# Kernel tuning notes

Measured on AMD Instinct MI355X. Metric: run time of the kernel, lower is better.

The kernel has to match this reference:

```python
import jax, jax.numpy as jnp
import numpy as np

B, T, E = 2, 2048, 1024
H = 16            # num_heads (global in source repo)
D = E // H        # head_len
LN_EPS = 1e-5


def setup_inputs() -> dict:
    key = jax.random.key(0)
    ks = jax.random.split(key, 12)
    s = lambda fan_in: 1.0 / np.sqrt(fan_in)
    return {
        "x":     jax.random.normal(ks[0], (B, T, E), jnp.float32),
        "ln1_g": jnp.ones((E,), jnp.float32),
        "ln1_b": jnp.zeros((E,), jnp.float32),
        "Wq":    jax.random.normal(ks[1], (E, E), jnp.float32) * s(E),
        "Wk":    jax.random.normal(ks[2], (E, E), jnp.float32) * s(E),
        "Wv":    jax.random.normal(ks[3], (E, E), jnp.float32) * s(E),
        "Wo":    jax.random.normal(ks[4], (E, E), jnp.float32) * s(E),
        "bo":    jnp.zeros((E,), jnp.float32),
        "ln2_g": jnp.ones((E,), jnp.float32),
        "ln2_b": jnp.zeros((E,), jnp.float32),
        "W1":    jax.random.normal(ks[5], (E, 4 * E), jnp.float32) * s(E),
        "b1":    jnp.zeros((4 * E,), jnp.float32),
        "W2":    jax.random.normal(ks[6], (4 * E, E), jnp.float32) * s(4 * E),
        "b2":    jnp.zeros((E,), jnp.float32),
    }


def _layernorm(x, g, b):
    mu = jnp.mean(x, axis=-1, keepdims=True)
    var = jnp.mean(jnp.square(x - mu), axis=-1, keepdims=True)
    return (x - mu) * jax.lax.rsqrt(var + LN_EPS) * g + b


def _attention(x, Wq, Wk, Wv, Wo, bo):
    b, t, e = x.shape
    q = (x @ Wq).reshape(b, t, H, D)
    k = (x @ Wk).reshape(b, t, H, D)
    v = (x @ Wv).reshape(b, t, H, D)
    scores = jnp.einsum("bqhd,bkhd->bhqk", q, k) / np.sqrt(D).astype(np.float32)
    causal = jnp.tril(jnp.ones((t, t), bool))
    scores = jnp.where(causal, scores, -jnp.inf)
    attn = jax.nn.softmax(scores, axis=-1)
    out = jnp.einsum("bhqk,bkhd->bqhd", attn, v).reshape(b, t, e)
    return out @ Wo + bo


def reference(x, ln1_g, ln1_b, Wq, Wk, Wv, Wo, bo, ln2_g, ln2_b, W1, b1, W2, b2):
    # pre-norm attention + residual (dropout=0 / eval mode)
    x = x + _attention(_layernorm(x, ln1_g, ln1_b), Wq, Wk, Wv, Wo, bo)
    # pre-norm MLP + residual
    h = _layernorm(x, ln2_g, ln2_b)
    h = jax.nn.relu(h @ W1 + b1) @ W2 + b2
    return x + h
```

## Files before the change

### kernel.cpp

```cpp
#include <hip/hip_runtime.h>
#include <cmath>
#include <cstdint>
#include <cstddef>

typedef __bf16 bf16_t;
typedef __bf16 bf16x8 __attribute__((ext_vector_type(8)));
typedef float  f32x4  __attribute__((ext_vector_type(4)));

#define B_   2
#define T_   2048
#define E_   1024
#define H_   16
#define D_   64
#define FF_  4096
#define NROW (B_ * T_)
#define QS_  (3 * E_)
#define NTI  (T_ / 64)

__global__ __launch_bounds__(256) void ln_kernel(
    const float* __restrict__ x, const float* __restrict__ g,
    const float* __restrict__ bta, bf16_t* __restrict__ out)
{
    int row = blockIdx.x;
    int tid = threadIdx.x;
    const float4* xr = (const float4*)(x + (size_t)row * E_);
    float4 v = xr[tid];
    float s  = v.x + v.y + v.z + v.w;
    float ss = v.x * v.x + v.y * v.y + v.z * v.z + v.w * v.w;
#pragma unroll
    for (int off = 32; off; off >>= 1) {
        s  += __shfl_xor(s, off);
        ss += __shfl_xor(ss, off);
    }
    __shared__ float red[8];
    int wave = tid >> 6, lane = tid & 63;
    if (lane == 0) { red[wave] = s; red[4 + wave] = ss; }
    __syncthreads();
    s  = red[0] + red[1] + red[2] + red[3];
    ss = red[4] + red[5] + red[6] + red[7];
    float mu   = s * (1.0f / E_);
    float var  = ss * (1.0f / E_) - mu * mu;
    float rstd = rsqrtf(var + 1e-5f);
    float4 gv = ((const float4*)g)[tid];
    float4 bv = ((const float4*)bta)[tid];
    union { bf16_t h[4]; ushort4 u; } pk;
    pk.h[0] = (bf16_t)((v.x - mu) * rstd * gv.x + bv.x);
    pk.h[1] = (bf16_t)((v.y - mu) * rstd * gv.y + bv.y);
    pk.h[2] = (bf16_t)((v.z - mu) * rstd * gv.z + bv.z);
    pk.h[3] = (bf16_t)((v.w - mu) * rstd * gv.w + bv.w);
    ((ushort4*)(out + (size_t)row * E_))[tid] = pk.u;
}

__global__ __launch_bounds__(256) void ln_reduce2(
    const float* __restrict__ p, const float* __restrict__ bias,
    const float* __restrict__ resid, float* __restrict__ x1,
    const float* __restrict__ g, const float* __restrict__ bta,
    bf16_t* __restrict__ out)
{
    int row = blockIdx.x;
    int tid = threadIdx.x;
    size_t off = (size_t)row * E_;
    float4 v0 = ((const float4*)(p + off))[tid];
    float4 v1 = ((const float4*)(p + (size_t)NROW * E_ + off))[tid];
    float4 bb = ((const float4*)bias)[tid];
    float4 rr = ((const float4*)(resid + off))[tid];
    float4 v;
    v.x = v0.x + v1.x + bb.x + rr.x;
    v.y = v0.y + v1.y + bb.y + rr.y;
    v.z = v0.z + v1.z + bb.z + rr.z;
    v.w = v0.w + v1.w + bb.w + rr.w;
    ((float4*)(x1 + off))[tid] = v;
    float s  = v.x + v.y + v.z + v.w;
    float ss = v.x * v.x + v.y * v.y + v.z * v.z + v.w * v.w;
#pragma unroll
    for (int o = 32; o; o >>= 1) {
        s  += __shfl_xor(s, o);
        ss += __shfl_xor(ss, o);
    }
    __shared__ float red[8];
    int wave = tid >> 6, lane = tid & 63;
    if (lane == 0) { red[wave] = s; red[4 + wave] = ss; }
    __syncthreads();
    s  = red[0] + red[1] + red[2] + red[3];
    ss = red[4] + red[5] + red[6] + red[7];
    float mu   = s * (1.0f / E_);
    float var  = ss * (1.0f / E_) - mu * mu;
    float rstd = rsqrtf(var + 1e-5f);
    float4 gv = ((const float4*)g)[tid];
    float4 bv = ((const float4*)bta)[tid];
    union { bf16_t h[4]; ushort4 u; } pk;
    pk.h[0] = (bf16_t)((v.x - mu) * rstd * gv.x + bv.x);
    pk.h[1] = (bf16_t)((v.y - mu) * rstd * gv.y + bv.y);
    pk.h[2] = (bf16_t)((v.z - mu) * rstd * gv.z + bv.z);
    pk.h[3] = (bf16_t)((v.w - mu) * rstd * gv.w + bv.w);
    ((ushort4*)(out + off))[tid] = pk.u;
}

__global__ __launch_bounds__(256) void add_reduce4(
    const float* __restrict__ p, const float* __restrict__ bias,
    const float* __restrict__ resid, float* __restrict__ out)
{
    int row = blockIdx.x;
    int tid = threadIdx.x;
    size_t off = (size_t)row * E_;
    const size_t MN = (size_t)NROW * E_;
    float4 v0 = ((const float4*)(p + off))[tid];
    float4 v1 = ((const float4*)(p + MN + off))[tid];
    float4 v2 = ((const float4*)(p + 2 * MN + off))[tid];
    float4 v3 = ((const float4*)(p + 3 * MN + off))[tid];
    float4 bb = ((const float4*)bias)[tid];
    float4 rr = ((const float4*)(resid + off))[tid];
    float4 v;
    v.x = (v0.x + v1.x) + (v2.x + v3.x) + bb.x + rr.x;
    v.y = (v0.y + v1.y) + (v2.y + v3.y) + bb.y + rr.y;
    v.z = (v0.z + v1.z) + (v2.z + v3.z) + bb.z + rr.z;
    v.w = (v0.w + v1.w) + (v2.w + v3.w) + bb.w + rr.w;
    ((float4*)(out + off))[tid] = v;
}

__global__ __launch_bounds__(256) void transpose_all(
    const float* __restrict__ Wq, const float* __restrict__ Wk,
    const float* __restrict__ Wv, const float* __restrict__ Wo,
    const float* __restrict__ W1, const float* __restrict__ W2,
    bf16_t* __restrict__ wqkv, bf16_t* __restrict__ wot,
    bf16_t* __restrict__ w1t, bf16_t* __restrict__ w2t)
{
    int l = blockIdx.x;
    const float* W; bf16_t* Wt; int K, N, bx, by;
    if (l < 4096) {
        int seg = l >> 10, r = l & 1023;
        K = E_; N = E_; bx = r & 31; by = r >> 5;
        if      (seg == 0) { W = Wq; Wt = wqkv; }
        else if (seg == 1) { W = Wk; Wt = wqkv + (size_t)E_ * E_; }
        else if (seg == 2) { W = Wv; Wt = wqkv + (size_t)2 * E_ * E_; }
        else               { W = Wo; Wt = wot; }
    } else if (l < 8192) {
        int r = l - 4096; K = E_; N = FF_; bx = r & 127; by = r >> 7;
        W = W1; Wt = w1t;
    } else {
        int r = l - 8192; K = FF_; N = E_; bx = r & 31; by = r >> 5;
        W = W2; Wt = w2t;
    }
    __shared__ float t[32][33];
    int n0 = bx * 32, k0 = by * 32;
    int tx = threadIdx.x & 31, ty = threadIdx.x >> 5;
#pragma unroll
    for (int i = 0; i < 4; ++i)
        t[ty + i * 8][tx] = W[(size_t)(k0 + ty + i * 8) * N + n0 + tx];
    __syncthreads();
#pragma unroll
    for (int i = 0; i < 4; ++i)
        Wt[(size_t)(n0 + ty + i * 8) * K + k0 + tx] = (bf16_t)t[tx][ty + i * 8];
}

#define BM 128
#define BN 128
#define BK 64

__device__ __forceinline__ void gload16(const bf16_t* g, bf16_t* l)
{
    __builtin_amdgcn_global_load_lds(
        (const __attribute__((address_space(1))) void*)g,
        (__attribute__((address_space(3))) void*)l, 16, 0, 0);
}

__global__ __launch_bounds__(256) void gemm_bt(
    const bf16_t* __restrict__ A, const bf16_t* __restrict__ Bt,
    const float* __restrict__ bias, const float* __restrict__ resid,
    void* __restrict__ Cout, bf16_t* __restrict__ vt_out,
    int M, int N, int K, int lda, int ldb,
    int has_bias, int do_relu, int has_resid, int out_bf16)
{
    __shared__ __attribute__((aligned(16))) bf16_t As[BM * BK];
    __shared__ __attribute__((aligned(16))) bf16_t Bs[BN * BK];
    int tid  = threadIdx.x;
    int lane = tid & 63, wave = tid >> 6;
    int m0 = blockIdx.x * BM, n0 = blockIdx.y * BN;
    int wm = (wave & 1) * 64, wn = (wave >> 1) * 64;
    int koff = blockIdx.z * K;
    f32x4 acc[4][4];
#pragma unroll
    for (int i = 0; i < 4; ++i)
#pragma unroll
        for (int j = 0; j < 4; ++j) acc[i][j] = (f32x4){0.f, 0.f, 0.f, 0.f};

    const int kq = (lane >> 4) * 8;
    const int ml = lane & 15;

    int srow = wave * 32 + (lane >> 3);
    int scol = (lane & 7) * 8;
    const bf16_t* Ag = A  + (size_t)(m0 + srow) * lda + koff + scol;
    const bf16_t* Bg = Bt + (size_t)(n0 + srow) * ldb + koff + scol;
    bf16_t* Asw = &As[wave * 32 * BK];
    bf16_t* Bsw = &Bs[wave * 32 * BK];
    int niter = K / BK;

#pragma unroll
    for (int j = 0; j < 4; ++j) {
        gload16(Ag + (size_t)j * 8 * lda, Asw + j * 8 * BK);
        gload16(Bg + (size_t)j * 8 * ldb, Bsw + j * 8 * BK);
    }

    for (int it = 0; it < niter; ++it) {
        __syncthreads();
#pragma unroll
        for (int ks = 0; ks < 2; ++ks) {
            bf16x8 af[4], bfr[4];
#pragma unroll
            for (int mi = 0; mi < 4; ++mi)
                af[mi] = *(const bf16x8*)&As[(wm + mi * 16 + ml) * BK + ks * 32 + kq];
#pragma unroll
            for (int ni = 0; ni < 4; ++ni)
                bfr[ni] = *(const bf16x8*)&Bs[(wn + ni * 16 + ml) * BK + ks * 32 + kq];
#pragma unroll
            for (int mi = 0; mi < 4; ++mi)
#pragma unroll
                for (int ni = 0; ni < 4; ++ni)
                    acc[mi][ni] = __builtin_amdgcn_mfma_f32_16x16x32_bf16(
                        af[mi], bfr[ni], acc[mi][ni], 0, 0, 0);
        }
        if (it + 1 < niter) {
            __syncthreads();
            int k0 = (it + 1) * BK;
#pragma unroll
            for (int j = 0; j < 4; ++j) {
                gload16(Ag + k0 + (size_t)j * 8 * lda, Asw + j * 8 * BK);
                gload16(Bg + k0 + (size_t)j * 8 * ldb, Bsw + j * 8 * BK);
            }
        }
    }

    int r4 = (lane >> 4) * 4;
    if (gridDim.z > 1) {
        float* P = (float*)Cout + (size_t)blockIdx.z * M * N;
#pragma unroll
        for (int mi = 0; mi < 4; ++mi)
#pragma unroll
            for (int ni = 0; ni < 4; ++ni) {
                int col = n0 + wn + ni * 16 + ml;
#pragma unroll
                for (int r = 0; r < 4; ++r) {
                    int row = m0 + wm + mi * 16 + r4 + r;
                    P[(size_t)row * N + col] = acc[mi][ni][r];
                }
            }
        return;
    }
#pragma unroll
    for (int mi = 0; mi < 4; ++mi) {
#pragma unroll
        for (int ni = 0; ni < 4; ++ni) {
            int col = n0 + wn + ni * 16 + ml;
            float bval = has_bias ? bias[col] : 0.0f;
#pragma unroll
            for (int r = 0; r < 4; ++r) {
                int row = m0 + wm + mi * 16 + r4 + r;
                float v = acc[mi][ni][r] + bval;
                if (do_relu)   v = fmaxf(v, 0.0f);
                if (has_resid) v += resid[(size_t)row * N + col];
                if (out_bf16)
                    ((bf16_t*)Cout)[(size_t)row * N + col] = (bf16_t)v;
                else
                    ((float*)Cout)[(size_t)row * N + col] = v;
            }
        }
    }
}


__device__ __forceinline__ void g256_stage_half(
    const bf16_t* gbase, int ldg, bf16_t* lhalf, int wave, int lane)
{
    int r = lane >> 3, c = lane & 7;
    int sc = (c ^ r) * 8;
#pragma unroll
    for (int j = 0; j < 2; ++j) {
        const bf16_t* src = gbase + (size_t)(wave * 8 + j * 64 + r) * ldg + sc;
        bf16_t* dst = lhalf + (wave * 8 + j * 64) * 64;
        __builtin_amdgcn_global_load_lds(
            (const __attribute__((address_space(1))) void*)src,
            (__attribute__((address_space(3))) void*)dst, 16, 0, 0);
    }
}

__device__ __forceinline__ bf16x8 g256_frag(const bf16_t* half, int row, int kb)
{
    return *(const bf16x8*)((const char*)half + row * 128 + (kb ^ ((row & 7) << 4)));
}

template<int FP, bool DO_BFR>
__device__ __forceinline__ void g256_reads(
    const bf16_t* Ahx, const bf16_t* Bhx,
    bf16x8 (&af)[2][2], bf16x8 (&bfr)[4][2],
    int ml, int kq16, int brow0)
{
    if (DO_BFR) {
#pragma unroll
        for (int ni = 0; ni < 4; ++ni) {
            bfr[ni][0] = g256_frag(Bhx, brow0 + ni * 16 + ml, kq16);
            bfr[ni][1] = g256_frag(Bhx, brow0 + ni * 16 + ml, 64 + kq16);
        }
    }
#pragma unroll
    for (int i = 0; i < 2; ++i) {
        af[i][0] = g256_frag(Ahx, (2 * FP + i) * 16 + ml, kq16);
        af[i][1] = g256_frag(Ahx, (2 * FP + i) * 16 + ml, 64 + kq16);
    }
}

template<int FP>
__device__ __forceinline__ void g256_mfma(
    const bf16x8 (&af)[2][2], const bf16x8 (&bfr)[4][2], f32x4 (&acc)[8][4])
{
    __builtin_amdgcn_s_setprio(1);
#pragma unroll
    for (int i = 0; i < 2; ++i)
#pragma unroll
        for (int ni = 0; ni < 4; ++ni)
#pragma unroll
            for (int ks = 0; ks < 2; ++ks)
                acc[2 * FP + i][ni] = __builtin_amdgcn_mfma_f32_16x16x32_bf16(
                    af[i][ks], bfr[ni][ks], acc[2 * FP + i][ni], 0, 0, 0);
    __builtin_amdgcn_s_setprio(0);
}

#define AHALF(t, h) (ldsr + ((((t) & 1) * 4 + (h)) * (128 * 64)))
#define BHALF(t, h) (ldsr + ((((t) & 1) * 4 + 2 + (h)) * (128 * 64)))
#define STG_A(t, h) g256_stage_half(Ab + (size_t)((h) * 128) * lda + (t) * 64, lda, AHALF(t, h), wave, lane)
#define STG_B(t, h) g256_stage_half(Bb + (size_t)((h) * 128) * ldb + (t) * 64, ldb, BHALF(t, h), wave, lane)
#define SBAR() __builtin_amdgcn_s_barrier()

__global__ __launch_bounds__(512, 2) void gemm256(
    const bf16_t* __restrict__ A, const bf16_t* __restrict__ Bt,
    const float* __restrict__ bias,
    void* __restrict__ Cout, bf16_t* __restrict__ vt_out,
    int M, int N, int K, int lda, int ldb,
    int has_bias, int do_relu, int split)
{
    extern __shared__ __attribute__((aligned(16))) bf16_t ldsr[];
    int tid = threadIdx.x, lane = tid & 63, wave = tid >> 6;
    int m0 = blockIdx.x * 256, n0 = blockIdx.y * 256;
    int koff = blockIdx.z * K;
    int ml = lane & 15, kq16 = (lane >> 4) * 16, r4 = (lane >> 4) * 4;
    int wr = (wave >> 2) * 128, wc = (wave & 3) * 64;
    int brow0 = (wave & 1) * 64;

    const bf16_t* Ab = A  + (size_t)m0 * lda + koff;
    const bf16_t* Bb = Bt + (size_t)n0 * ldb + koff;

    const bf16_t* A0 = AHALF(0, wave >> 2);
    const bf16_t* A1 = AHALF(1, wave >> 2);
    const bf16_t* B0 = BHALF(0, (wave & 3) >> 1);
    const bf16_t* B1 = BHALF(1, (wave & 3) >> 1);

    f32x4 acc[8][4];
#pragma unroll
    for (int i = 0; i < 8; ++i)
#pragma unroll
        for (int j = 0; j < 4; ++j) acc[i][j] = (f32x4){0.f, 0.f, 0.f, 0.f};
    bf16x8 bfr[4][2];

    STG_B(0, 0); STG_B(0, 1);
    STG_A(0, 0); STG_A(0, 1);
    STG_B(1, 0); STG_B(1, 1);
    asm volatile("s_waitcnt vmcnt(4)" ::: "memory");
    SBAR();

    int NIT2 = K / 128;
    for (int it = 0; it < NIT2; ++it) {
        bool last = (it == NIT2 - 1);
        int t1 = 2 * it + 1, t2 = 2 * it + 2, t3 = 2 * it + 3;
        bf16x8 af[2][2];

        g256_reads<0, true>(A0, B0, af, bfr, ml, kq16, brow0);
        STG_A(t1, 0);
        SBAR();
        g256_mfma<0>(af, bfr, acc);
        SBAR();

        g256_reads<1, false>(A0, B0, af, bfr, ml, kq16, brow0);
        STG_A(t1, 1);
        SBAR();
        g256_mfma<1>(af, bfr, acc);
        SBAR();

        g256_reads<2, false>(A0, B0, af, bfr, ml, kq16, brow0);
        if (!last) STG_B(t2, 0);
        SBAR();
        g256_mfma<2>(af, bfr, acc);
        SBAR();

        g256_reads<3, false>(A0, B0, af, bfr, ml, kq16, brow0);
        if (!last) STG_B(t2, 1);
        SBAR();
        g256_mfma<3>(af, bfr, acc);
        if (last) asm volatile("s_waitcnt vmcnt(0)" ::: "memory");
        else      asm volatile("s_waitcnt vmcnt(4)" ::: "memory");
        SBAR();

        g256_reads<0, true>(A1, B1, af, bfr, ml, kq16, brow0);
        if (!last) STG_A(t2, 0);
        SBAR();
        g256_mfma<0>(af, bfr, acc);
        SBAR();

        g256_reads<1, false>(A1, B1, af, bfr, ml, kq16, brow0);
        if (!last) STG_A(t2, 1);
        SBAR();
        g256_mfma<1>(af, bfr, acc);
        SBAR();

        g256_reads<2, false>(A1, B1, af, bfr, ml, kq16, brow0);
        if (!last) STG_B(t3, 0);
        SBAR();
        g256_mfma<2>(af, bfr, acc);
        SBAR();

        g256_reads<3, false>(A1, B1, af, bfr, ml, kq16, brow0);
        if (!last) STG_B(t3, 1);
        SBAR();
        g256_mfma<3>(af, bfr, acc);
        if (!last) asm volatile("s_waitcnt vmcnt(4)" ::: "memory");
        SBAR();
    }

    if (split > 1) {
        float* P = (float*)Cout + (size_t)blockIdx.z * M * N;
#pragma unroll
        for (int mi = 0; mi < 8; ++mi)
#pragma unroll
            for (int ni = 0; ni < 4; ++ni) {
                int col = n0 + wc + ni * 16 + ml;
#pragma unroll
                for (int r = 0; r < 4; ++r) {
                    int row = m0 + wr + mi * 16 + r4 + r;
                    P[(size_t)row * N + col] = acc[mi][ni][r];
                }
            }
        return;
    }
    if (vt_out && n0 >= 2 * E_) {
#pragma unroll
        for (int mi = 0; mi < 8; ++mi)
#pragma unroll
            for (int ni = 0; ni < 4; ++ni) {
                int vcol = n0 + wc + ni * 16 + ml - 2 * E_;
                int h = vcol >> 6, d = vcol & 63;
                int row0 = m0 + wr + mi * 16 + r4;
                int b = row0 >> 11, t = row0 & (T_ - 1);
                union { bf16_t h4[4]; uint2 u; } pk;
#pragma unroll
                for (int r = 0; r < 4; ++r) pk.h4[r] = (bf16_t)acc[mi][ni][r];
                *(uint2*)&vt_out[((size_t)(b * H_ + h) * D_ + d) * T_ + t] = pk.u;
            }
        return;
    }
#pragma unroll
    for (int mi = 0; mi < 8; ++mi) {
#pragma unroll
        for (int ni = 0; ni < 4; ++ni) {
            int col = n0 + wc + ni * 16 + ml;
            float bval = has_bias ? bias[col] : 0.0f;
#pragma unroll
            for (int r = 0; r < 4; ++r) {
                int row = m0 + wr + mi * 16 + r4 + r;
                float v = acc[mi][ni][r] + bval;
                if (do_relu) v = fmaxf(v, 0.0f);
                ((bf16_t*)Cout)[(size_t)row * N + col] = (bf16_t)v;
            }
        }
    }
}

#define PSTR 72

struct TileState {
    f32x4 acc[4];
    float m1, l1;
};

__device__ __forceinline__ void tile_update(
    const bf16x8 kf[2][4], const bf16x8 vf[2][4], const bf16x8 qf[2],
    TileState& st, bf16_t* PsW, int ml, int r4, int kq8,
    bool diag, int ch, int qrow)
{
    f32x4 s[4];
#pragma unroll
    for (int nt = 0; nt < 4; ++nt) {
        s[nt] = (f32x4){0.f, 0.f, 0.f, 0.f};
#pragma unroll
        for (int ks = 0; ks < 2; ++ks)
            s[nt] = __builtin_amdgcn_mfma_f32_16x16x32_bf16(kf[ks][nt], qf[ks], s[nt], 0, 0, 0);
    }
    if (diag) {
#pragma unroll
        for (int nt = 0; nt < 4; ++nt)
#pragma unroll
            for (int r = 0; r < 4; ++r)
                if (ch * 64 + nt * 16 + r4 + r > qrow) s[nt][r] = -INFINITY;
    }
    float mx = -INFINITY;
#pragma unroll
    for (int nt = 0; nt < 4; ++nt)
#pragma unroll
        for (int r = 0; r < 4; ++r) mx = fmaxf(mx, s[nt][r]);
    mx = fmaxf(mx, __shfl_xor(mx, 16));
    mx = fmaxf(mx, __shfl_xor(mx, 32));
    float mn = fmaxf(st.m1, mx);
    float al = __expf(st.m1 - mn);
    st.m1 = mn;
    float sum = 0.f;
#pragma unroll
    for (int nt = 0; nt < 4; ++nt)
#pragma unroll
        for (int r = 0; r < 4; ++r) {
            float p = __expf(s[nt][r] - mn);
            s[nt][r] = p;
            sum += p;
        }
    sum += __shfl_xor(sum, 16);
    sum += __shfl_xor(sum, 32);
    st.l1 = st.l1 * al + sum;
#pragma unroll
    for (int dt = 0; dt < 4; ++dt)
#pragma unroll
        for (int r = 0; r < 4; ++r) st.acc[dt][r] *= al;

#pragma unroll
    for (int nt = 0; nt < 4; ++nt) {
        union { bf16_t h[4]; uint2 u; } pk;
#pragma unroll
        for (int r = 0; r < 4; ++r) pk.h[r] = (bf16_t)s[nt][r];
        *(uint2*)&PsW[ml * PSTR + nt * 16 + r4] = pk.u;
    }
#pragma unroll
    for (int ks = 0; ks < 2; ++ks) {
        bf16x8 pf = *(const bf16x8*)&PsW[ml * PSTR + ks * 32 + kq8];
#pragma unroll
        for (int dt = 0; dt < 4; ++dt)
            st.acc[dt] = __builtin_amdgcn_mfma_f32_16x16x32_bf16(vf[ks][dt], pf, st.acc[dt], 0, 0, 0);
    }
}

__global__ __launch_bounds__(256) void attn_mfma(
    const bf16_t* __restrict__ Qp, const bf16_t* __restrict__ Kp,
    const bf16_t* __restrict__ Vt, bf16_t* __restrict__ O)
{
    __shared__ __attribute__((aligned(16))) bf16_t Ks[2][64 * PSTR];
    __shared__ __attribute__((aligned(16))) bf16_t Vts[2][64 * PSTR];
    __shared__ __attribute__((aligned(16))) bf16_t Ps[4][16 * PSTR];

    int tid = threadIdx.x, lane = tid & 63, wave = tid >> 6;
    int ml  = lane & 15;
    int kq8 = (lane >> 4) * 8;
    int r4  = (lane >> 4) * 4;
    int bh = blockIdx.y, b = bh >> 4, h = bh & 15;
    size_t qk_base = (size_t)b * T_ * QS_ + h * D_;
    size_t vt_base = (size_t)bh * D_ * T_;
    size_t o_base  = (size_t)b * T_ * E_ + h * D_;

    int lo = blockIdx.x, hi = NTI - 1 - blockIdx.x;
    int qlo = lo * 64 + wave * 16;
    int qhi = hi * 64 + wave * 16;

    bf16x8 qfl[2], qfh[2];
#pragma unroll
    for (int ks = 0; ks < 2; ++ks) {
        bf16x8 a = *(const bf16x8*)&Qp[qk_base + (size_t)(qlo + ml) * QS_ + ks * 32 + kq8];
        bf16x8 c = *(const bf16x8*)&Qp[qk_base + (size_t)(qhi + ml) * QS_ + ks * 32 + kq8];
#pragma unroll
        for (int j = 0; j < 8; ++j) {
            a[j] = (bf16_t)((float)a[j] * 0.125f);
            c[j] = (bf16_t)((float)c[j] * 0.125f);
        }
        qfl[ks] = a; qfh[ks] = c;
    }

    TileState stl, sth;
#pragma unroll
    for (int dt = 0; dt < 4; ++dt) {
        stl.acc[dt] = (f32x4){0.f, 0.f, 0.f, 0.f};
        sth.acc[dt] = (f32x4){0.f, 0.f, 0.f, 0.f};
    }
    stl.m1 = -INFINITY; stl.l1 = 0.f;
    sth.m1 = -INFINITY; sth.l1 = 0.f;

    int r0 = tid >> 3, c0 = (tid & 7) * 8;
    int nch = hi + 1;

    {
        const bf16_t* kb = &Kp[qk_base + (size_t)r0 * QS_ + c0];
        const bf16_t* vb = &Vt[vt_base + (size_t)r0 * T_ + c0];
        uint4 k0v = *(const uint4*)kb;
        uint4 k1v = *(const uint4*)(kb + (size_t)32 * QS_);
        uint4 v0v = *(const uint4*)vb;
        uint4 v1v = *(const uint4*)(vb + (size_t)32 * T_);
        *(uint4*)&Ks[0][r0 * PSTR + c0]         = k0v;
        *(uint4*)&Ks[0][(r0 + 32) * PSTR + c0]  = k1v;
        *(uint4*)&Vts[0][r0 * PSTR + c0]        = v0v;
        *(uint4*)&Vts[0][(r0 + 32) * PSTR + c0] = v1v;
    }

    for (int ch = 0; ch < nch; ++ch) {
        int cur = ch & 1, nxt = cur ^ 1;
        __syncthreads();

        uint4 nk0, nk1, nv0, nv1;
        bool pf = (ch + 1 < nch);
        if (pf) {
            const bf16_t* kb = &Kp[qk_base + (size_t)((ch + 1) * 64 + r0) * QS_ + c0];
            const bf16_t* vb = &Vt[vt_base + (size_t)r0 * T_ + (ch + 1) * 64 + c0];
            nk0 = *(const uint4*)kb;
            nk1 = *(const uint4*)(kb + (size_t)32 * QS_);
            nv0 = *(const uint4*)vb;
            nv1 = *(const uint4*)(vb + (size_t)32 * T_);
        }

        bf16x8 kf[2][4], vf[2][4];
#pragma unroll
        for (int ks = 0; ks < 2; ++ks)
#pragma unroll
            for (int nt = 0; nt < 4; ++nt) {
                kf[ks][nt] = *(const bf16x8*)&Ks[cur][(nt * 16 + ml) * PSTR + ks * 32 + kq8];
                vf[ks][nt] = *(const bf16x8*)&Vts[cur][(nt * 16 + ml) * PSTR + ks * 32 + kq8];
            }

        tile_update(kf, vf, qfh, sth, Ps[wave], ml, r4, kq8,
                    ch == hi, ch, qhi + ml);
        if (ch <= lo)
            tile_update(kf, vf, qfl, stl, Ps[wave], ml, r4, kq8,
                        ch == lo, ch, qlo + ml);

        if (pf) {
            *(uint4*)&Ks[nxt][r0 * PSTR + c0]         = nk0;
            *(uint4*)&Ks[nxt][(r0 + 32) * PSTR + c0]  = nk1;
            *(uint4*)&Vts[nxt][r0 * PSTR + c0]        = nv0;
            *(uint4*)&Vts[nxt][(r0 + 32) * PSTR + c0] = nv1;
        }
    }

#pragma unroll
    for (int t = 0; t < 2; ++t) {
        TileState& st = t ? stl : sth;
        int qw = t ? qlo : qhi;
        float inv = 1.0f / st.l1;
#pragma unroll
        for (int dt = 0; dt < 4; ++dt) {
            union { bf16_t h[4]; uint2 u; } pk;
#pragma unroll
            for (int r = 0; r < 4; ++r) pk.h[r] = (bf16_t)(st.acc[dt][r] * inv);
            *(uint2*)&Ps[wave][ml * PSTR + dt * 16 + r4] = pk.u;
        }
        int row = lane >> 2, seg = (lane & 3) * 16;
        bf16x8 o0 = *(const bf16x8*)&Ps[wave][row * PSTR + seg];
        bf16x8 o1 = *(const bf16x8*)&Ps[wave][row * PSTR + seg + 8];
        size_t gp = o_base + (size_t)(qw + row) * E_ + seg;
        *(bf16x8*)&O[gp]     = o0;
        *(bf16x8*)&O[gp + 8] = o1;
    }
}

extern "C" void kernel_launch(void* const* d_in, const int* in_sizes, int n_in,
                              void* d_out, int out_size, void* d_ws, size_t ws_size,
                              hipStream_t stream)
{
    const float* x    = (const float*)d_in[0];
    const float* ln1g = (const float*)d_in[1];
    const float* ln1b = (const float*)d_in[2];
    const float* Wq   = (const float*)d_in[3];
    const float* Wk   = (const float*)d_in[4];
    const float* Wv   = (const float*)d_in[5];
    const float* Wo   = (const float*)d_in[6];
    const float* bo   = (const float*)d_in[7];
    const float* ln2g = (const float*)d_in[8];
    const float* ln2b = (const float*)d_in[9];
    const float* W1   = (const float*)d_in[10];
    const float* b1   = (const float*)d_in[11];
    const float* W2   = (const float*)d_in[12];
    const float* b2   = (const float*)d_in[13];

    char* ws = (char*)d_ws;
    const size_t MB = 1024ull * 1024ull;
    bf16_t* w2t     = (bf16_t*)(ws + 0 * MB);
    float*  x1      = (float*)(ws + 8 * MB);
    float*  part_wo = (float*)(ws + 24 * MB);
    bf16_t* h1      = (bf16_t*)(ws + 24 * MB);
    bf16_t* w1t     = (bf16_t*)(ws + 56 * MB);
    bf16_t* xn      = (bf16_t*)(ws + 64 * MB);
    bf16_t* hb      = (bf16_t*)(ws + 64 * MB);
    bf16_t* wqkv    = (bf16_t*)(ws + 72 * MB);
    bf16_t* wot     = (bf16_t*)(ws + 78 * MB);
    bf16_t* QKV     = (bf16_t*)(ws + 80 * MB);
    bf16_t* Vtb     = (bf16_t*)(ws + 104 * MB);
    bf16_t* att     = (bf16_t*)(ws + 112 * MB);
    float*  part4   = (float*)(ws + 56 * MB);

    dim3 blk(256), blk5(512);
    const size_t LDS256 = 8 * 128 * 64 * sizeof(bf16_t);

    transpose_all<<<dim3(12288), blk, 0, stream>>>(
        Wq, Wk, Wv, Wo, W1, W2, wqkv, wot, w1t, w2t);

    ln_kernel<<<dim3(NROW), blk, 0, stream>>>(x, ln1g, ln1b, xn);

    gemm256<<<dim3(NROW / 256, QS_ / 256, 1), blk5, LDS256, stream>>>(
        xn, wqkv, nullptr, QKV, Vtb, NROW, QS_, E_, E_, E_, 0, 0, 1);

    attn_mfma<<<dim3(NTI / 2, B_ * H_), blk, 0, stream>>>(
        QKV, QKV + E_, Vtb, att);

    gemm_bt<<<dim3(NROW / BM, E_ / BN, 2), blk, 0, stream>>>(
        att, wot, nullptr, nullptr, part_wo, nullptr, NROW, E_, E_ / 2, E_, E_, 0, 0, 0, 0);
    ln_reduce2<<<dim3(NROW), blk, 0, stream>>>(
        part_wo, bo, x, x1, ln2g, ln2b, hb);

    gemm256<<<dim3(NROW / 256, FF_ / 256, 1), blk5, LDS256, stream>>>(
        hb, w1t, b1, h1, nullptr, NROW, FF_, E_, E_, E_, 1, 1, 1);

    gemm256<<<dim3(NROW / 256, E_ / 256, 4), blk5, LDS256, stream>>>(
        h1, w2t, nullptr, part4, nullptr, NROW, E_, FF_ / 4, FF_, FF_, 0, 0, 4);
    add_reduce4<<<dim3(NROW), blk, 0, stream>>>(
        part4, b2, x1, (float*)d_out);
}
```

Baseline: 333.2 us.

## Use direct global-to-LDS swizzled loads and lazy softmax rescale in attention

The generic GEMM and the attention kernel now stage tiles with global_load_lds into XOR-swizzled LDS layouts instead of padded layouts. In attention this replaces the register round-trip prefetch, so the next K/V chunk lands asynchronously while the current one is computed. Tile_update gains s_setprio around the MFMA blocks, a tree max reduction, and skips rescaling the accumulator unless the running max grows by more than a threshold. The two query tiles also get separate P scratch buffers. The lazy rescale lets exponents reach up to e^8 before renormalising, which slightly changes numerics in exchange for fewer multiplies.

```diff
diff --git a/kernel.cpp b/kernel.cpp
--- a/kernel.cpp
+++ b/kernel.cpp
@@ -153,16 +153,16 @@
         Wt[(size_t)(n0 + ty + i * 8) * K + k0 + tx] = (bf16_t)t[tx][ty + i * 8];
 }
 
+__device__ __forceinline__ void gload16(const bf16_t* g, bf16_t* l)
+{
+    __builtin_amdgcn_global_load_lds(
+        (const __attribute__((address_space(1))) void*)g,
+        (__attribute__((address_space(3))) void*)l, 16, 0, 0);
+}
+
 #define BM 128
 #define BN 128
 #define BK 64
-
-__device__ __forceinline__ void gload16(const bf16_t* g, bf16_t* l)
-{
-    __builtin_amdgcn_global_load_lds(
-        (const __attribute__((address_space(1))) void*)g,
-        (__attribute__((address_space(3))) void*)l, 16, 0, 0);
-}
 
 __global__ __launch_bounds__(256) void gemm_bt(
     const bf16_t* __restrict__ A, const bf16_t* __restrict__ Bt,
@@ -184,13 +184,14 @@
 #pragma unroll
         for (int j = 0; j < 4; ++j) acc[i][j] = (f32x4){0.f, 0.f, 0.f, 0.f};
 
-    const int kq = (lane >> 4) * 8;
     const int ml = lane & 15;
-
-    int srow = wave * 32 + (lane >> 3);
-    int scol = (lane & 7) * 8;
-    const bf16_t* Ag = A  + (size_t)(m0 + srow) * lda + koff + scol;
-    const bf16_t* Bg = Bt + (size_t)(n0 + srow) * ldb + koff + scol;
+    const int g  = lane >> 4;
+    const int swl = ml & 7;
+
+    int r8 = lane >> 3;
+    int scw = ((lane & 7) ^ r8) * 8;
+    const bf16_t* Ag = A  + (size_t)(m0 + wave * 32 + r8) * lda + koff + scw;
+    const bf16_t* Bg = Bt + (size_t)(n0 + wave * 32 + r8) * ldb + koff + scw;
     bf16_t* Asw = &As[wave * 32 * BK];
     bf16_t* Bsw = &Bs[wave * 32 * BK];
     int niter = K / BK;
@@ -201,17 +202,20 @@
         gload16(Bg + (size_t)j * 8 * ldb, Bsw + j * 8 * BK);
     }
 
+    const char* Ac = (const char*)As;
+    const char* Bc = (const char*)Bs;
     for (int it = 0; it < niter; ++it) {
         __syncthreads();
 #pragma unroll
         for (int ks = 0; ks < 2; ++ks) {
+            int swc = (((ks << 2) + g) ^ swl) << 4;
             bf16x8 af[4], bfr[4];
 #pragma unroll
             for (int mi = 0; mi < 4; ++mi)
-                af[mi] = *(const bf16x8*)&As[(wm + mi * 16 + ml) * BK + ks * 32 + kq];
+                af[mi] = *(const bf16x8*)(Ac + (wm + mi * 16 + ml) * 128 + swc);
 #pragma unroll
             for (int ni = 0; ni < 4; ++ni)
-                bfr[ni] = *(const bf16x8*)&Bs[(wn + ni * 16 + ml) * BK + ks * 32 + kq];
+                bfr[ni] = *(const bf16x8*)(Bc + (wn + ni * 16 + ml) * 128 + swc);
 #pragma unroll
             for (int mi = 0; mi < 4; ++mi)
 #pragma unroll
@@ -267,7 +271,6 @@
     }
 }
 
-
 __device__ __forceinline__ void g256_stage_half(
     const bf16_t* gbase, int ldg, bf16_t* lhalf, int wave, int lane)
 {
@@ -479,12 +482,27 @@
     float m1, l1;
 };
 
+__device__ __forceinline__ void attn_stage(
+    const bf16_t* kb, const bf16_t* vb,
+    bf16_t* ksl, bf16_t* vsl, int wave, int lane)
+{
+    int r = lane >> 3;
+    int sc = ((lane & 7) ^ r) * 8;
+#pragma unroll
+    for (int j = 0; j < 2; ++j) {
+        int rb = wave * 16 + j * 8;
+        gload16(kb + (size_t)(rb + r) * QS_ + sc, ksl + rb * 64);
+        gload16(vb + (size_t)(rb + r) * T_  + sc, vsl + rb * 64);
+    }
+}
+
 __device__ __forceinline__ void tile_update(
     const bf16x8 kf[2][4], const bf16x8 vf[2][4], const bf16x8 qf[2],
     TileState& st, bf16_t* PsW, int ml, int r4, int kq8,
     bool diag, int ch, int qrow)
 {
     f32x4 s[4];
+    __builtin_amdgcn_s_setprio(1);
 #pragma unroll
     for (int nt = 0; nt < 4; ++nt) {
         s[nt] = (f32x4){0.f, 0.f, 0.f, 0.f};
@@ -492,6 +510,7 @@
         for (int ks = 0; ks < 2; ++ks)
             s[nt] = __builtin_amdgcn_mfma_f32_16x16x32_bf16(kf[ks][nt], qf[ks], s[nt], 0, 0, 0);
     }
+    __builtin_amdgcn_s_setprio(0);
     if (diag) {
 #pragma unroll
         for (int nt = 0; nt < 4; ++nt)
@@ -499,32 +518,37 @@
             for (int r = 0; r < 4; ++r)
                 if (ch * 64 + nt * 16 + r4 + r > qrow) s[nt][r] = -INFINITY;
     }
-    float mx = -INFINITY;
-#pragma unroll
-    for (int nt = 0; nt < 4; ++nt)
-#pragma unroll
-        for (int r = 0; r < 4; ++r) mx = fmaxf(mx, s[nt][r]);
+    float t0 = fmaxf(fmaxf(s[0][0], s[0][1]), s[0][2]);
+    float t1 = fmaxf(fmaxf(s[0][3], s[1][0]), s[1][1]);
+    float t2 = fmaxf(fmaxf(s[1][2], s[1][3]), s[2][0]);
+    float t3 = fmaxf(fmaxf(s[2][1], s[2][2]), s[2][3]);
+    float t4 = fmaxf(fmaxf(s[3][0], s[3][1]), s[3][2]);
+    float mx = fmaxf(fmaxf(fmaxf(t0, t1), t2),
+                     fmaxf(fmaxf(t3, t4), s[3][3]));
     mx = fmaxf(mx, __shfl_xor(mx, 16));
     mx = fmaxf(mx, __shfl_xor(mx, 32));
-    float mn = fmaxf(st.m1, mx);
-    float al = __expf(st.m1 - mn);
-    st.m1 = mn;
+    if (!__all(mx - st.m1 <= 8.0f)) {
+        float mn = fmaxf(st.m1, mx);
+        float al = __expf(st.m1 - mn);
+        st.m1 = mn;
+        st.l1 *= al;
+#pragma unroll
+        for (int dt = 0; dt < 4; ++dt)
+#pragma unroll
+            for (int r = 0; r < 4; ++r) st.acc[dt][r] *= al;
+    }
     float sum = 0.f;
 #pragma unroll
     for (int nt = 0; nt < 4; ++nt)
 #pragma unroll
         for (int r = 0; r < 4; ++r) {
-            float p = __expf(s[nt][r] - mn);
+            float p = __expf(s[nt][r] - st.m1);
             s[nt][r] = p;
             sum += p;
         }
     sum += __shfl_xor(sum, 16);
     sum += __shfl_xor(sum, 32);
-    st.l1 = st.l1 * al + sum;
-#pragma unroll
-    for (int dt = 0; dt < 4; ++dt)
-#pragma unroll
-        for (int r = 0; r < 4; ++r) st.acc[dt][r] *= al;
+    st.l1 += sum;
 
 #pragma unroll
     for (int nt = 0; nt < 4; ++nt) {
@@ -533,6 +557,7 @@
         for (int r = 0; r < 4; ++r) pk.h[r] = (bf16_t)s[nt][r];
         *(uint2*)&PsW[ml * PSTR + nt * 16 + r4] = pk.u;
     }
+    __builtin_amdgcn_s_setprio(1);
 #pragma unroll
     for (int ks = 0; ks < 2; ++ks) {
         bf16x8 pf = *(const bf16x8*)&PsW[ml * PSTR + ks * 32 + kq8];
@@ -540,20 +565,23 @@
         for (int dt = 0; dt < 4; ++dt)
             st.acc[dt] = __builtin_amdgcn_mfma_f32_16x16x32_bf16(vf[ks][dt], pf, st.acc[dt], 0, 0, 0);
     }
+    __builtin_amdgcn_s_setprio(0);
 }
 
 __global__ __launch_bounds__(256) void attn_mfma(
     const bf16_t* __restrict__ Qp, const bf16_t* __restrict__ Kp,
     const bf16_t* __restrict__ Vt, bf16_t* __restrict__ O)
 {
-    __shared__ __attribute__((aligned(16))) bf16_t Ks[2][64 * PSTR];
-    __shared__ __attribute__((aligned(16))) bf16_t Vts[2][64 * PSTR];
-    __shared__ __attribute__((aligned(16))) bf16_t Ps[4][16 * PSTR];
+    __shared__ __attribute__((aligned(16))) bf16_t Ks[2][64 * 64];
+    __shared__ __attribute__((aligned(16))) bf16_t Vts[2][64 * 64];
+    __shared__ __attribute__((aligned(16))) bf16_t Ps[8][16 * PSTR];
 
     int tid = threadIdx.x, lane = tid & 63, wave = tid >> 6;
     int ml  = lane & 15;
     int kq8 = (lane >> 4) * 8;
+    int g   = lane >> 4;
     int r4  = (lane >> 4) * 4;
+    int swl = ml & 7;
     int bh = blockIdx.y, b = bh >> 4, h = bh & 15;
     size_t qk_base = (size_t)b * T_ * QS_ + h * D_;
     size_t vt_base = (size_t)bh * D_ * T_;
@@ -585,75 +613,56 @@
     stl.m1 = -INFINITY; stl.l1 = 0.f;
     sth.m1 = -INFINITY; sth.l1 = 0.f;
 
-    int r0 = tid >> 3, c0 = (tid & 7) * 8;
     int nch = hi + 1;
 
-    {
-        const bf16_t* kb = &Kp[qk_base + (size_t)r0 * QS_ + c0];
-        const bf16_t* vb = &Vt[vt_base + (size_t)r0 * T_ + c0];
-        uint4 k0v = *(const uint4*)kb;
-        uint4 k1v = *(const uint4*)(kb + (size_t)32 * QS_);
-        uint4 v0v = *(const uint4*)vb;
-        uint4 v1v = *(const uint4*)(vb + (size_t)32 * T_);
-        *(uint4*)&Ks[0][r0 * PSTR + c0]         = k0v;
-        *(uint4*)&Ks[0][(r0 + 32) * PSTR + c0]  = k1v;
-        *(uint4*)&Vts[0][r0 * PSTR + c0]        = v0v;
-        *(uint4*)&Vts[0][(r0 + 32) * PSTR + c0] = v1v;
-    }
+    attn_stage(Kp + qk_base, Vt + vt_base, Ks[0], Vts[0], wave, lane);
 
     for (int ch = 0; ch < nch; ++ch) {
         int cur = ch & 1, nxt = cur ^ 1;
         __syncthreads();
 
-        uint4 nk0, nk1, nv0, nv1;
-        bool pf = (ch + 1 < nch);
-        if (pf) {
-            const bf16_t* kb = &Kp[qk_base + (size_t)((ch + 1) * 64 + r0) * QS_ + c0];
-            const bf16_t* vb = &Vt[vt_base + (size_t)r0 * T_ + (ch + 1) * 64 + c0];
-            nk0 = *(const uint4*)kb;
-            nk1 = *(const uint4*)(kb + (size_t)32 * QS_);
-            nv0 = *(const uint4*)vb;
-            nv1 = *(const uint4*)(vb + (size_t)32 * T_);
-        }
+        if (ch + 1 < nch)
+            attn_stage(Kp + qk_base + (size_t)((ch + 1) * 64) * QS_,
+                       Vt + vt_base + (ch + 1) * 64,
+                       Ks[nxt], Vts[nxt], wave, lane);
 
         bf16x8 kf[2][4], vf[2][4];
-#pragma unroll
-        for (int ks = 0; ks < 2; ++ks)
+        const char* kc = (const char*)Ks[cur];
+        const char* vc = (const char*)Vts[cur];
+#pragma unroll
+        for (int ks = 0; ks < 2; ++ks) {
+            int swc = (((ks << 2) + g) ^ swl) << 4;
 #pragma unroll
             for (int nt = 0; nt < 4; ++nt) {
-                kf[ks][nt] = *(const bf16x8*)&Ks[cur][(nt * 16 + ml) * PSTR + ks * 32 + kq8];
-                vf[ks][nt] = *(const bf16x8*)&Vts[cur][(nt * 16 + ml) * PSTR + ks * 32 + kq8];
+                int off = (nt * 16 + ml) * 128 + swc;
+                kf[ks][nt] = *(const bf16x8*)(kc + off);
+                vf[ks][nt] = *(const bf16x8*)(vc + off);
             }
+        }
 
         tile_update(kf, vf, qfh, sth, Ps[wave], ml, r4, kq8,
                     ch == hi, ch, qhi + ml);
         if (ch <= lo)
-            tile_update(kf, vf, qfl, stl, Ps[wave], ml, r4, kq8,
+            tile_update(kf, vf, qfl, stl, Ps[wave + 4], ml, r4, kq8,
                         ch == lo, ch, qlo + ml);
-
-        if (pf) {
-            *(uint4*)&Ks[nxt][r0 * PSTR + c0]         = nk0;
-            *(uint4*)&Ks[nxt][(r0 + 32) * PSTR + c0]  = nk1;
-            *(uint4*)&Vts[nxt][r0 * PSTR + c0]        = nv0;
-            *(uint4*)&Vts[nxt][(r0 + 32) * PSTR + c0] = nv1;
-        }
     }
 
 #pragma unroll
     for (int t = 0; t < 2; ++t) {
         TileState& st = t ? stl : sth;
         int qw = t ? qlo : qhi;
+        bf16_t* PsW = Ps[wave + (t ? 4 : 0)];
         float inv = 1.0f / st.l1;
 #pragma unroll
         for (int dt = 0; dt < 4; ++dt) {
             union { bf16_t h[4]; uint2 u; } pk;
 #pragma unroll
             for (int r = 0; r < 4; ++r) pk.h[r] = (bf16_t)(st.acc[dt][r] * inv);
-            *(uint2*)&Ps[wave][ml * PSTR + dt * 16 + r4] = pk.u;
+            *(uint2*)&PsW[ml * PSTR + dt * 16 + r4] = pk.u;
         }
         int row = lane >> 2, seg = (lane & 3) * 16;
-        bf16x8 o0 = *(const bf16x8*)&Ps[wave][row * PSTR + seg];
-        bf16x8 o1 = *(const bf16x8*)&Ps[wave][row * PSTR + seg + 8];
+        bf16x8 o0 = *(const bf16x8*)&PsW[row * PSTR + seg];
+        bf16x8 o1 = *(const bf16x8*)&PsW[row * PSTR + seg + 8];
         size_t gp = o_base + (size_t)(qw + row) * E_ + seg;
         *(bf16x8*)&O[gp]     = o0;
         *(bf16x8*)&O[gp + 8] = o1;
```

After: 329.7 us. Within noise of the previous version (-1.0%).
